# Optimization experiments

Hardware: AMD Instinct MI355X
Metric: run time of the kernel (lower is better)

Reference implementation:

```python
import jax, jax.numpy as jnp
import numpy as np

B, T, C = 1, 2048, 2048
H, KH, HD = 16, 4, 128  # n_head, n_kv_head, head_dim
ROPE_BASE = 10000.0


def setup_inputs() -> dict:
    key = jax.random.key(0)
    ks = jax.random.split(key, 5)
    s = 0.02
    return {
        "x": jax.random.normal(ks[0], (B, T, C), jnp.float32),
        "Wq": jax.random.normal(ks[1], (C, H * HD), jnp.float32) * s,
        "Wk": jax.random.normal(ks[2], (C, KH * HD), jnp.float32) * s,
        "Wv": jax.random.normal(ks[3], (C, KH * HD), jnp.float32) * s,
        "Wo": jax.random.normal(ks[4], (H * HD, C), jnp.float32) * s,
        "position_ids": jnp.arange(T, dtype=jnp.int32),
    }


def _rotate_half(a):
    h = a.shape[-1] // 2
    return jnp.concatenate([-a[..., h:], a[..., :h]], axis=-1)


def reference(x, Wq, Wk, Wv, Wo, position_ids):
    b, t, c = x.shape
    n_rep = H // KH
    # projections -> [B, heads, T, HD]
    q = (x @ Wq).reshape(b, t, H, HD).transpose(0, 2, 1, 3)
    k = (x @ Wk).reshape(b, t, KH, HD).transpose(0, 2, 1, 3)
    v = (x @ Wv).reshape(b, t, KH, HD).transpose(0, 2, 1, 3)
    # rotary embedding cache [T, HD]
    inv_freq = 1.0 / (ROPE_BASE ** (jnp.arange(0, HD, 2, dtype=jnp.float32) / HD))
    pos = jnp.arange(t, dtype=jnp.float32)
    freqs = pos[:, None] * inv_freq[None, :]
    emb = jnp.concatenate([freqs, freqs], axis=-1)
    cos = jnp.cos(emb)[position_ids][None, None]  # [1,1,T,HD]
    sin = jnp.sin(emb)[position_ids][None, None]
    q = q * cos + _rotate_half(q) * sin
    k = k * cos + _rotate_half(k) * sin
    # GQA: group query heads instead of materializing repeated K/V
    qg = q.reshape(b, KH, n_rep, t, HD)
    scale = jnp.float32(1.0 / np.sqrt(HD))
    scores = jnp.einsum('bgrtd,bgsd->bgrts', qg, k) * scale
    causal = jnp.tril(jnp.ones((t, t), dtype=bool))
    scores = jnp.where(causal, scores, jnp.float32(-1e30))
    p = jax.nn.softmax(scores, axis=-1)
    y = jnp.einsum('bgrts,bgsd->bgrtd', p, v)
    y = y.reshape(b, H, t, HD).transpose(0, 2, 1, 3).reshape(b, t, H * HD)
    return y @ Wo
```

## Files before the change

### kernel.cpp

```cpp
#include <hip/hip_runtime.h>

typedef unsigned short u16;
using bf16x8 = __attribute__((ext_vector_type(8))) short;
using f32x4  = __attribute__((ext_vector_type(4))) float;

#define GLD16(g, l)                                                            \
  __builtin_amdgcn_global_load_lds(                                            \
      (const __attribute__((address_space(1))) void*)(g),                      \
      (__attribute__((address_space(3))) void*)(l), 16, 0, 0)

__device__ __forceinline__ u16 f2b(float x) {
  union { float f; unsigned u; } v; v.f = x;
  unsigned r = v.u + 0x7FFF + ((v.u >> 16) & 1);
  return (u16)(r >> 16);
}
__device__ __forceinline__ float b2f(u16 x) {
  union { unsigned u; float f; } v; v.u = (unsigned)x << 16; return v.f;
}

__global__ void prep_kernel(const float* __restrict__ x,
                            const float* __restrict__ Wq,
                            const float* __restrict__ Wk,
                            const float* __restrict__ Wv,
                            const float* __restrict__ Wo,
                            const int* __restrict__ pos, u16* __restrict__ xb,
                            float2* __restrict__ tbl, u16* __restrict__ Wqkv_bt,
                            u16* __restrict__ Wo_bt) {
  __shared__ float tile[32][33];
  const int b = blockIdx.x, tid = threadIdx.x;
  if (b < 10240) {
    const int bx = b % 160, k0 = (b / 160) * 32;
    const int tx = tid & 31, ty = tid >> 5;
    const float* src; int srcN, n0s; u16* dst; int dstRow0;
    if (bx < 64)      { src = Wq; srcN = 2048; n0s = bx * 32;        dst = Wqkv_bt; dstRow0 = bx * 32; }
    else if (bx < 80) { src = Wk; srcN = 512;  n0s = (bx - 64) * 32; dst = Wqkv_bt; dstRow0 = 2048 + (bx - 64) * 32; }
    else if (bx < 96) { src = Wv; srcN = 512;  n0s = (bx - 80) * 32; dst = Wqkv_bt; dstRow0 = 2560 + (bx - 80) * 32; }
    else              { src = Wo; srcN = 2048; n0s = (bx - 96) * 32; dst = Wo_bt;   dstRow0 = (bx - 96) * 32; }
#pragma unroll
    for (int r = 0; r < 4; r++)
      tile[ty + r * 8][tx] = src[(size_t)(k0 + ty + r * 8) * srcN + n0s + tx];
    __syncthreads();
#pragma unroll
    for (int r = 0; r < 4; r++)
      dst[(size_t)(dstRow0 + ty + r * 8) * 2048 + k0 + tx] = f2b(tile[tx][ty + r * 8]);
  } else {
    int gid = (b - 10240) * 256 + tid;
    const float c0 = -0.015625f * 13.287712379549449f;
    for (int j = gid; j < 2048 * 64; j += 262144) {
      int t = j >> 6, d = j & 63;
      float ang = (float)pos[t] * exp2f((float)d * c0);
      tbl[j] = make_float2(cosf(ang), sinf(ang));
    }
    for (int i = gid; i < 1048576; i += 262144) {
      float4 v = ((const float4*)x)[i];
      ushort4 o;
      o.x = f2b(v.x); o.y = f2b(v.y); o.z = f2b(v.z); o.w = f2b(v.w);
      ((ushort4*)xb)[i] = o;
    }
  }
}

__global__ __launch_bounds__(256, 2)
void gemm_qkv_rope(const u16* __restrict__ A, const u16* __restrict__ Bt,
                   const float2* __restrict__ tbl, u16* __restrict__ Qb,
                   u16* __restrict__ Kb, u16* __restrict__ Vtb) {
  __shared__ u16 lds_[8][128 * 32];
  const int K = 2048;
  const int tid = threadIdx.x;
  const int lane = tid & 63;
  const int w = tid >> 6;
  const int wr = w >> 1, wc = w & 1;
  const int m0 = blockIdx.y * 128, n0 = blockIdx.x * 128;

  f32x4 acc[4][4] = {};

  const int srow = tid >> 2, skg = tid & 3;
  const u16* Ag0 = A + (size_t)(m0 + srow) * K + skg * 8;
  const u16* Ag1 = A + (size_t)(m0 + 64 + srow) * K + skg * 8;
  const u16* Bg0 = Bt + (size_t)(n0 + srow) * K + skg * 8;
  const u16* Bg1 = Bt + (size_t)(n0 + 64 + srow) * K + skg * 8;

  const int l0 = tid * 8, l1 = (256 + tid) * 8;
  u16 *pa0 = lds_[0], *pa1 = lds_[1], *pa2 = lds_[2], *pa3 = lds_[3];
  u16 *pb0 = lds_[4], *pb1 = lds_[5], *pb2 = lds_[6], *pb3 = lds_[7];

#define GSTAGE(k0v, pa, pb)                                                    \
  {                                                                            \
    GLD16(Ag0 + (k0v), (pa) + l0);                                             \
    GLD16(Ag1 + (k0v), (pa) + l1);                                             \
    GLD16(Bg0 + (k0v), (pb) + l0);                                             \
    GLD16(Bg1 + (k0v), (pb) + l1);                                             \
  }

  GSTAGE(0, pa0, pb0);
  GSTAGE(32, pa1, pb1);

  const int frow = lane & 15, fk = (lane >> 4) * 8;
  const int nk = K >> 5;

  for (int i = 0; i < nk; ++i) {
    if (i + 2 < nk) {
      GSTAGE((i + 2) * 32, pa2, pb2);
      asm volatile("s_waitcnt vmcnt(8)" ::: "memory");
    } else if (i + 1 < nk) {
      asm volatile("s_waitcnt vmcnt(4)" ::: "memory");
    } else {
      asm volatile("s_waitcnt vmcnt(0)" ::: "memory");
    }
    __builtin_amdgcn_s_barrier();
    __builtin_amdgcn_sched_barrier(0);
    bf16x8 av[4], bv[4];
#pragma unroll
    for (int m = 0; m < 4; m++)
      av[m] = *(const bf16x8*)(pa0 + (wr * 64 + m * 16 + frow) * 32 + fk);
#pragma unroll
    for (int n = 0; n < 4; n++)
      bv[n] = *(const bf16x8*)(pb0 + (wc * 64 + n * 16 + frow) * 32 + fk);
#pragma unroll
    for (int m = 0; m < 4; m++)
#pragma unroll
      for (int n = 0; n < 4; n++)
        acc[m][n] =
            __builtin_amdgcn_mfma_f32_16x16x32_bf16(av[m], bv[n], acc[m][n], 0, 0, 0);
    u16* t;
    t = pa0; pa0 = pa1; pa1 = pa2; pa2 = pa3; pa3 = t;
    t = pb0; pb0 = pb1; pb1 = pb2; pb2 = pb3; pb3 = t;
  }
#undef GSTAGE

  const int crow = (lane >> 4) * 4, ccol = lane & 15;
  __syncthreads();
  float* S = (float*)lds_;
#pragma unroll
  for (int m = 0; m < 4; m++)
#pragma unroll
    for (int n = 0; n < 4; n++)
#pragma unroll
      for (int r = 0; r < 4; r++)
        S[(wr * 64 + m * 16 + crow + r) * 128 + wc * 64 + n * 16 + ccol] =
            acc[m][n][r];
  __syncthreads();
  if (n0 < 2560) {
    const bool isQ = (n0 < 2048);
    u16* dst = isQ ? Qb + (size_t)(n0 >> 7) * 2048 * 128
                   : Kb + (size_t)((n0 - 2048) >> 7) * 2048 * 128;
    const float sgn = (wc == 0) ? -1.f : 1.f;
    const float qs = isQ ? 0.08838834764831845f : 1.0f;
#pragma unroll
    for (int m = 0; m < 4; m++)
#pragma unroll
      for (int n = 0; n < 4; n++)
#pragma unroll
        for (int r = 0; r < 4; r++) {
          int row = wr * 64 + m * 16 + crow + r;
          int col = wc * 64 + n * 16 + ccol;
          int t = m0 + row, d = col & 63;
          float2 cs = tbl[t * 64 + d];
          float val = acc[m][n][r] * cs.x + sgn * S[row * 128 + (col ^ 64)] * cs.y;
          dst[(size_t)t * 128 + col] = f2b(val * qs);
        }
  } else {
    const int g = (n0 - 2560) >> 7;
    u16* dst = Vtb + (size_t)g * 128 * 2048;
    const int d = tid >> 1, th = (tid & 1) * 64;
#pragma unroll
    for (int j = 0; j < 8; j++) {
      bf16x8 v;
#pragma unroll
      for (int e = 0; e < 8; e++) v[e] = (short)f2b(S[(th + j * 8 + e) * 128 + d]);
      *(bf16x8*)(dst + (size_t)d * 2048 + m0 + th + j * 8) = v;
    }
  }
}

__global__ __launch_bounds__(256, 2)
void gemm_bt_128(const u16* __restrict__ A, const u16* __restrict__ Bt,
                 float* __restrict__ C, int M, int N, int K) {
  __shared__ u16 As[4][128 * 32];
  __shared__ u16 Bs[4][128 * 32];
  const int tid = threadIdx.x;
  const int lane = tid & 63;
  const int w = tid >> 6;
  const int wr = w >> 1, wc = w & 1;
  const int m0 = blockIdx.y * 128, n0 = blockIdx.x * 128;

  f32x4 acc[4][4] = {};

  const int srow = tid >> 2, skg = tid & 3;
  const u16* Ag0 = A + (size_t)(m0 + srow) * K + skg * 8;
  const u16* Ag1 = A + (size_t)(m0 + 64 + srow) * K + skg * 8;
  const u16* Bg0 = Bt + (size_t)(n0 + srow) * K + skg * 8;
  const u16* Bg1 = Bt + (size_t)(n0 + 64 + srow) * K + skg * 8;

  const int l0 = tid * 8, l1 = (256 + tid) * 8;
  u16 *pa0 = As[0], *pa1 = As[1], *pa2 = As[2], *pa3 = As[3];
  u16 *pb0 = Bs[0], *pb1 = Bs[1], *pb2 = Bs[2], *pb3 = Bs[3];

#define GSTAGE(k0v, pa, pb)                                                    \
  {                                                                            \
    GLD16(Ag0 + (k0v), (pa) + l0);                                             \
    GLD16(Ag1 + (k0v), (pa) + l1);                                             \
    GLD16(Bg0 + (k0v), (pb) + l0);                                             \
    GLD16(Bg1 + (k0v), (pb) + l1);                                             \
  }

  GSTAGE(0, pa0, pb0);
  GSTAGE(32, pa1, pb1);

  const int frow = lane & 15, fk = (lane >> 4) * 8;
  const int nk = K >> 5;

  for (int i = 0; i < nk; ++i) {
    if (i + 2 < nk) {
      GSTAGE((i + 2) * 32, pa2, pb2);
      asm volatile("s_waitcnt vmcnt(8)" ::: "memory");
    } else if (i + 1 < nk) {
      asm volatile("s_waitcnt vmcnt(4)" ::: "memory");
    } else {
      asm volatile("s_waitcnt vmcnt(0)" ::: "memory");
    }
    __builtin_amdgcn_s_barrier();
    __builtin_amdgcn_sched_barrier(0);
    bf16x8 av[4], bv[4];
#pragma unroll
    for (int m = 0; m < 4; m++)
      av[m] = *(const bf16x8*)(pa0 + (wr * 64 + m * 16 + frow) * 32 + fk);
#pragma unroll
    for (int n = 0; n < 4; n++)
      bv[n] = *(const bf16x8*)(pb0 + (wc * 64 + n * 16 + frow) * 32 + fk);
#pragma unroll
    for (int m = 0; m < 4; m++)
#pragma unroll
      for (int n = 0; n < 4; n++)
        acc[m][n] =
            __builtin_amdgcn_mfma_f32_16x16x32_bf16(av[m], bv[n], acc[m][n], 0, 0, 0);
    u16* t;
    t = pa0; pa0 = pa1; pa1 = pa2; pa2 = pa3; pa3 = t;
    t = pb0; pb0 = pb1; pb1 = pb2; pb2 = pb3; pb3 = t;
  }
#undef GSTAGE

  const int crow = (lane >> 4) * 4, ccol = lane & 15;
#pragma unroll
  for (int m = 0; m < 4; m++)
#pragma unroll
    for (int n = 0; n < 4; n++)
#pragma unroll
      for (int r = 0; r < 4; r++)
        C[(size_t)(m0 + wr * 64 + m * 16 + crow + r) * N +
          (n0 + wc * 64 + n * 16 + ccol)] = acc[m][n][r];
}

__global__ __launch_bounds__(256, 3)
void attn_kernel(const u16* __restrict__ Qb, const u16* __restrict__ Kb,
                 const u16* __restrict__ Vtb, u16* __restrict__ op0,
                 u16* __restrict__ op1, u16* __restrict__ op2,
                 float* __restrict__ ml) {
  __shared__ u16 Ks[64 * 128];
  __shared__ u16 Vs[128 * 64];
  __shared__ u16 Ps[4][16 * 64];
  const int tid = threadIdx.x, lane = tid & 63, w = tid >> 6;
  const int h = blockIdx.y, g = h >> 2;
  const int z = blockIdx.z;
  const int frow = lane & 15, fgrp = lane >> 4;
  const int t0 = blockIdx.x;
  const int t1 = 31 - t0;
  const int c0 = (t0 >= z) ? (t0 - z) / 3 + 1 : 0;
  const int c1 = (t1 - z) / 3 + 1;
  const int nit = c0 + c1;
  u16* myOp = (z == 0) ? op0 : (z == 1) ? op1 : op2;

  const u16* Kg = Kb + (size_t)g * 2048 * 128;
  const u16* Vg = Vtb + (size_t)g * 128 * 2048;

#define STAGE(j0v)                                                             \
  {                                                                            \
    _Pragma("unroll")                                                          \
    for (int i = 0; i < 4; i++) {                                              \
      int p = tid + i * 256;                                                   \
      int kr = p >> 4, kc = (p & 15) ^ (kr & 7);                               \
      GLD16(Kg + (size_t)((j0v) + kr) * 128 + kc * 8, Ks + p * 8);             \
      int vr = p >> 3, vc = (p & 7) ^ (vr & 7);                                \
      GLD16(Vg + (size_t)vr * 2048 + (j0v) + vc * 8, Vs + p * 8);              \
    }                                                                          \
  }

#define FLUSH()                                                                \
  {                                                                            \
    _Pragma("unroll")                                                          \
    for (int r = 0; r < 4; r++) {                                              \
      float inv = lrow[r] > 0.f ? 1.0f / lrow[r] : 0.f;                        \
      int t = qw + fgrp * 4 + r;                                               \
      _Pragma("unroll")                                                        \
      for (int db = 0; db < 8; db++)                                           \
        myOp[(size_t)t * 2048 + h * 128 + db * 16 + frow] = f2b(o[db][r] * inv);\
      if (frow == 0) {                                                         \
        int mi = (((z * 16 + h) * 2048) + t) * 2;                              \
        ml[mi] = mrow[r]; ml[mi + 1] = lrow[r];                                \
      }                                                                        \
    }                                                                          \
  }

  int qw = t0 * 64 + w * 16;
  bf16x8 qf[4];
  {
    const u16* Qrow = Qb + ((size_t)h * 2048 + (qw + frow)) * 128 + fgrp * 8;
#pragma unroll
    for (int kf = 0; kf < 4; kf++) qf[kf] = *(const bf16x8*)(Qrow + kf * 32);
  }

  f32x4 o[8] = {};
  float mrow[4], lrow[4];
#pragma unroll
  for (int r = 0; r < 4; r++) { mrow[r] = -1e30f; lrow[r] = 0.f; }

  for (int it = 0; it < nit; ++it) {
    const int pass = (it < c0) ? 0 : 1;
    const int j = (pass == 0) ? z + 3 * it : z + 3 * (it - c0);
    STAGE(j * 64);
    if (it == c0) {
      FLUSH();
#pragma unroll
      for (int db = 0; db < 8; db++)
#pragma unroll
        for (int r = 0; r < 4; r++) o[db][r] = 0.f;
#pragma unroll
      for (int r = 0; r < 4; r++) { mrow[r] = -1e30f; lrow[r] = 0.f; }
      qw = t1 * 64 + w * 16;
      const u16* Qrow = Qb + ((size_t)h * 2048 + (qw + frow)) * 128 + fgrp * 8;
#pragma unroll
      for (int kf = 0; kf < 4; kf++) qf[kf] = *(const bf16x8*)(Qrow + kf * 32);
    }
    __syncthreads();
    const bool diag = (pass == 0) ? (j == t0) : (j == t1);

    f32x4 sc[4] = {};
#pragma unroll
    for (int c = 0; c < 4; c++)
#pragma unroll
      for (int kf = 0; kf < 4; kf++) {
        int row = c * 16 + frow;
        bf16x8 kv = *(const bf16x8*)(
            &Ks[row * 128 + ((kf * 4 + fgrp) ^ (row & 7)) * 8]);
        sc[c] = __builtin_amdgcn_mfma_f32_16x16x32_bf16(qf[kf], kv, sc[c], 0, 0, 0);
      }
    if (diag) {
#pragma unroll
      for (int c = 0; c < 4; c++) {
        int jj = c * 16 + frow;
#pragma unroll
        for (int r = 0; r < 4; r++)
          if (jj > (w * 16 + fgrp * 4 + r)) sc[c][r] = -1e30f;
      }
    }
    float pm[4];
#pragma unroll
    for (int r = 0; r < 4; r++)
      pm[r] = fmaxf(fmaxf(sc[0][r], sc[1][r]), fmaxf(sc[2][r], sc[3][r]));
#pragma unroll
    for (int off = 1; off < 16; off <<= 1)
#pragma unroll
      for (int r = 0; r < 4; r++) pm[r] = fmaxf(pm[r], __shfl_xor(pm[r], off, 64));
    bool nd = false;
#pragma unroll
    for (int r = 0; r < 4; r++) nd = nd || (pm[r] > mrow[r] + 8.f);
    if (__any(nd)) {
#pragma unroll
      for (int r = 0; r < 4; r++) {
        float mn = fmaxf(mrow[r], pm[r]);
        float alpha = __expf(mrow[r] - mn);
        mrow[r] = mn;
        lrow[r] *= alpha;
#pragma unroll
        for (int db = 0; db < 8; db++) o[db][r] *= alpha;
      }
    }
    float rs[4];
#pragma unroll
    for (int r = 0; r < 4; r++) {
      float s = 0.f;
#pragma unroll
      for (int c = 0; c < 4; c++) { sc[c][r] = __expf(sc[c][r] - mrow[r]); s += sc[c][r]; }
      rs[r] = s;
    }
#pragma unroll
    for (int off = 1; off < 16; off <<= 1)
#pragma unroll
      for (int r = 0; r < 4; r++) rs[r] += __shfl_xor(rs[r], off, 64);
#pragma unroll
    for (int r = 0; r < 4; r++) lrow[r] += rs[r];
    u16* Pw = Ps[w];
#pragma unroll
    for (int c = 0; c < 4; c++)
#pragma unroll
      for (int r = 0; r < 4; r++) {
        int row = fgrp * 4 + r, col = c * 16 + frow;
        Pw[row * 64 + (((col >> 3) ^ row) & 7) * 8 + (col & 7)] = f2b(sc[c][r]);
      }
    asm volatile("s_waitcnt lgkmcnt(0)" ::: "memory");
    bf16x8 pf[2];
#pragma unroll
    for (int ks = 0; ks < 2; ks++)
      pf[ks] = *(const bf16x8*)(
          &Pw[frow * 64 + ((ks * 4 + fgrp) ^ (frow & 7)) * 8]);
#pragma unroll
    for (int db = 0; db < 8; db++)
#pragma unroll
      for (int ks = 0; ks < 2; ks++) {
        int row = db * 16 + frow;
        bf16x8 vf = *(const bf16x8*)(
            &Vs[row * 64 + ((ks * 4 + fgrp) ^ (row & 7)) * 8]);
        o[db] = __builtin_amdgcn_mfma_f32_16x16x32_bf16(pf[ks], vf, o[db], 0, 0, 0);
      }
    __syncthreads();
  }
  FLUSH();
#undef STAGE
#undef FLUSH
}

__global__ void attn_combine_kernel(const u16* __restrict__ op0,
                                    const u16* __restrict__ op1,
                                    const u16* __restrict__ op2,
                                    const float* __restrict__ ml,
                                    u16* __restrict__ Y) {
  int u = blockIdx.x * blockDim.x + threadIdx.x;
  int t = u >> 4, h = u & 15;
  float m0 = ml[((0 + h) * 2048 + t) * 2],       l0 = ml[((0 + h) * 2048 + t) * 2 + 1];
  float m1 = ml[((16 + h) * 2048 + t) * 2],      l1 = ml[((16 + h) * 2048 + t) * 2 + 1];
  float m2 = ml[((32 + h) * 2048 + t) * 2],      l2 = ml[((32 + h) * 2048 + t) * 2 + 1];
  float m = fmaxf(fmaxf(m0, m1), m2);
  float w0 = __expf(m0 - m) * l0, w1 = __expf(m1 - m) * l1, w2 = __expf(m2 - m) * l2;
  float inv = 1.0f / (w0 + w1 + w2);
  w0 *= inv; w1 *= inv; w2 *= inv;
  size_t base = (size_t)t * 2048 + h * 128;
#pragma unroll
  for (int i = 0; i < 16; i++) {
    bf16x8 a = *(const bf16x8*)(op0 + base + i * 8);
    bf16x8 b = *(const bf16x8*)(op1 + base + i * 8);
    bf16x8 c = *(const bf16x8*)(op2 + base + i * 8);
    bf16x8 out;
#pragma unroll
    for (int jj = 0; jj < 8; jj++)
      out[jj] = (short)f2b(w0 * b2f((u16)a[jj]) + w1 * b2f((u16)b[jj]) +
                           w2 * b2f((u16)c[jj]));
    *(bf16x8*)(Y + base + i * 8) = out;
  }
}

extern "C" void kernel_launch(void* const* d_in, const int* in_sizes, int n_in,
                              void* d_out, int out_size, void* d_ws,
                              size_t ws_size, hipStream_t stream) {
  const float* x  = (const float*)d_in[0];
  const float* Wq = (const float*)d_in[1];
  const float* Wk = (const float*)d_in[2];
  const float* Wv = (const float*)d_in[3];
  const float* Wo = (const float*)d_in[4];
  const int* pos  = (const int*)d_in[5];
  float* out = (float*)d_out;
  char* ws = (char*)d_ws;

  u16* xb      = (u16*)(ws + 0);
  u16* Wqkv_bt = (u16*)(ws + 8388608);
  u16* Wo_bt   = (u16*)(ws + 20971520);
  float2* tbl  = (float2*)(ws + 29360128);
  u16* Yb      = (u16*)(ws + 31457280);
  u16* Op2     = (u16*)(ws + 39845888);
  u16* Qb      = (u16*)(ws + 54525952);
  u16* Kb      = (u16*)(ws + 62914560);
  u16* Vtb     = (u16*)(ws + 67108864);
  u16* Op0     = (u16*)(ws + 0);
  u16* Op1     = (u16*)(ws + 8388608);
  float* ml    = (float*)(ws + 16777216);

  prep_kernel<<<11264, 256, 0, stream>>>(x, Wq, Wk, Wv, Wo, pos, xb, tbl,
                                         Wqkv_bt, Wo_bt);

  gemm_qkv_rope<<<dim3(24, 16), 256, 0, stream>>>(xb, Wqkv_bt, tbl, Qb, Kb, Vtb);

  attn_kernel<<<dim3(16, 16, 3), 256, 0, stream>>>(Qb, Kb, Vtb, Op0, Op1, Op2, ml);
  attn_combine_kernel<<<128, 256, 0, stream>>>(Op0, Op1, Op2, ml, Yb);

  gemm_bt_128<<<dim3(16, 16), 256, 0, stream>>>(Yb, Wo_bt, out, 2048, 2048, 2048);
}
```

Baseline: 243.1 us.

## Double query rows per attention wave and split KV four ways

Each wave now processes 32 query rows (two 16-row MFMA fragments) against each staged K/V tile, so a block covers 128 queries and every LDS K/V load is reused twice. The KV split along the sequence goes from 3 to 4 partitions, with a fourth partial output buffer and a 4-way combine, and the grid becomes 8x16x4. The point is to halve K/V staging and LDS traffic per unit of attention work. In exchange register pressure roughly doubles (launch bounds drop to 2 blocks per SM), more diagonal tiles need masking, and the combine reads an extra partial buffer. The workspace layout is also reorganised.

```diff
diff --git a/kernel.cpp b/kernel.cpp
--- a/kernel.cpp
+++ b/kernel.cpp
@@ -251,25 +251,25 @@
           (n0 + wc * 64 + n * 16 + ccol)] = acc[m][n][r];
 }
 
-__global__ __launch_bounds__(256, 3)
+__global__ __launch_bounds__(256, 2)
 void attn_kernel(const u16* __restrict__ Qb, const u16* __restrict__ Kb,
                  const u16* __restrict__ Vtb, u16* __restrict__ op0,
                  u16* __restrict__ op1, u16* __restrict__ op2,
-                 float* __restrict__ ml) {
+                 u16* __restrict__ op3, float* __restrict__ ml) {
   __shared__ u16 Ks[64 * 128];
   __shared__ u16 Vs[128 * 64];
-  __shared__ u16 Ps[4][16 * 64];
+  __shared__ u16 Ps[4][32 * 64];
   const int tid = threadIdx.x, lane = tid & 63, w = tid >> 6;
   const int h = blockIdx.y, g = h >> 2;
   const int z = blockIdx.z;
   const int frow = lane & 15, fgrp = lane >> 4;
   const int t0 = blockIdx.x;
-  const int t1 = 31 - t0;
-  const int c0 = (t0 >= z) ? (t0 - z) / 3 + 1 : 0;
-  const int c1 = (t1 - z) / 3 + 1;
+  const int t1 = 15 - t0;
+  const int c0 = (2 * t0 + 1 >= z) ? (2 * t0 + 1 - z) / 4 + 1 : 0;
+  const int c1 = (2 * t1 + 1 - z) / 4 + 1;
   const int nit = c0 + c1;
-  u16* myOp = (z == 0) ? op0 : (z == 1) ? op1 : op2;
-
+
+  u16* myOp = (z == 0) ? op0 : (z == 1) ? op1 : (z == 2) ? op2 : op3;
   const u16* Kg = Kb + (size_t)g * 2048 * 128;
   const u16* Vg = Vtb + (size_t)g * 128 * 2048;
 
@@ -288,53 +288,72 @@
 #define FLUSH()                                                                \
   {                                                                            \
     _Pragma("unroll")                                                          \
-    for (int r = 0; r < 4; r++) {                                              \
-      float inv = lrow[r] > 0.f ? 1.0f / lrow[r] : 0.f;                        \
-      int t = qw + fgrp * 4 + r;                                               \
+    for (int rg = 0; rg < 2; rg++)                                             \
       _Pragma("unroll")                                                        \
-      for (int db = 0; db < 8; db++)                                           \
-        myOp[(size_t)t * 2048 + h * 128 + db * 16 + frow] = f2b(o[db][r] * inv);\
-      if (frow == 0) {                                                         \
-        int mi = (((z * 16 + h) * 2048) + t) * 2;                              \
-        ml[mi] = mrow[r]; ml[mi + 1] = lrow[r];                                \
+      for (int r = 0; r < 4; r++) {                                            \
+        float lr = rg ? lrow1[r] : lrow0[r];                                   \
+        float mr = rg ? mrow1[r] : mrow0[r];                                   \
+        float inv = lr > 0.f ? 1.0f / lr : 0.f;                                \
+        int t = qw + rg * 16 + fgrp * 4 + r;                                   \
+        _Pragma("unroll")                                                      \
+        for (int db = 0; db < 8; db++) {                                       \
+          float ov = rg ? o1[db][r] : o0[db][r];                               \
+          myOp[(size_t)t * 2048 + h * 128 + db * 16 + frow] = f2b(ov * inv);   \
+        }                                                                      \
+        if (frow == 0) {                                                       \
+          int mi = (((z * 16 + h) * 2048) + t) * 2;                            \
+          ml[mi] = mr; ml[mi + 1] = lr;                                        \
+        }                                                                      \
       }                                                                        \
-    }                                                                          \
-  }
-
-  int qw = t0 * 64 + w * 16;
-  bf16x8 qf[4];
+  }
+
+  int qw = t0 * 128 + w * 32;
+  bf16x8 qf0[4], qf1[4];
   {
-    const u16* Qrow = Qb + ((size_t)h * 2048 + (qw + frow)) * 128 + fgrp * 8;
-#pragma unroll
-    for (int kf = 0; kf < 4; kf++) qf[kf] = *(const bf16x8*)(Qrow + kf * 32);
-  }
-
-  f32x4 o[8] = {};
-  float mrow[4], lrow[4];
-#pragma unroll
-  for (int r = 0; r < 4; r++) { mrow[r] = -1e30f; lrow[r] = 0.f; }
+    const u16* Qr0 = Qb + ((size_t)h * 2048 + (qw + frow)) * 128 + fgrp * 8;
+    const u16* Qr1 = Qb + ((size_t)h * 2048 + (qw + 16 + frow)) * 128 + fgrp * 8;
+#pragma unroll
+    for (int kf = 0; kf < 4; kf++) {
+      qf0[kf] = *(const bf16x8*)(Qr0 + kf * 32);
+      qf1[kf] = *(const bf16x8*)(Qr1 + kf * 32);
+    }
+  }
+
+  f32x4 o0[8] = {}, o1[8] = {};
+  float mrow0[4], lrow0[4], mrow1[4], lrow1[4];
+#pragma unroll
+  for (int r = 0; r < 4; r++) {
+    mrow0[r] = -1e30f; lrow0[r] = 0.f; mrow1[r] = -1e30f; lrow1[r] = 0.f;
+  }
 
   for (int it = 0; it < nit; ++it) {
     const int pass = (it < c0) ? 0 : 1;
-    const int j = (pass == 0) ? z + 3 * it : z + 3 * (it - c0);
+    const int j = (pass == 0) ? z + 4 * it : z + 4 * (it - c0);
     STAGE(j * 64);
     if (it == c0) {
       FLUSH();
 #pragma unroll
       for (int db = 0; db < 8; db++)
 #pragma unroll
-        for (int r = 0; r < 4; r++) o[db][r] = 0.f;
-#pragma unroll
-      for (int r = 0; r < 4; r++) { mrow[r] = -1e30f; lrow[r] = 0.f; }
-      qw = t1 * 64 + w * 16;
-      const u16* Qrow = Qb + ((size_t)h * 2048 + (qw + frow)) * 128 + fgrp * 8;
-#pragma unroll
-      for (int kf = 0; kf < 4; kf++) qf[kf] = *(const bf16x8*)(Qrow + kf * 32);
+        for (int r = 0; r < 4; r++) { o0[db][r] = 0.f; o1[db][r] = 0.f; }
+#pragma unroll
+      for (int r = 0; r < 4; r++) {
+        mrow0[r] = -1e30f; lrow0[r] = 0.f; mrow1[r] = -1e30f; lrow1[r] = 0.f;
+      }
+      qw = t1 * 128 + w * 32;
+      const u16* Qr0 = Qb + ((size_t)h * 2048 + (qw + frow)) * 128 + fgrp * 8;
+      const u16* Qr1 = Qb + ((size_t)h * 2048 + (qw + 16 + frow)) * 128 + fgrp * 8;
+#pragma unroll
+      for (int kf = 0; kf < 4; kf++) {
+        qf0[kf] = *(const bf16x8*)(Qr0 + kf * 32);
+        qf1[kf] = *(const bf16x8*)(Qr1 + kf * 32);
+      }
     }
     __syncthreads();
-    const bool diag = (pass == 0) ? (j == t0) : (j == t1);
-
-    f32x4 sc[4] = {};
+    const int qt = (pass == 0) ? t0 : t1;
+    const bool diag = (j >= 2 * qt);
+
+    f32x4 sc0[4] = {}, sc1[4] = {};
 #pragma unroll
     for (int c = 0; c < 4; c++)
 #pragma unroll
@@ -342,67 +361,89 @@
         int row = c * 16 + frow;
         bf16x8 kv = *(const bf16x8*)(
             &Ks[row * 128 + ((kf * 4 + fgrp) ^ (row & 7)) * 8]);
-        sc[c] = __builtin_amdgcn_mfma_f32_16x16x32_bf16(qf[kf], kv, sc[c], 0, 0, 0);
+        sc0[c] = __builtin_amdgcn_mfma_f32_16x16x32_bf16(qf0[kf], kv, sc0[c], 0, 0, 0);
+        sc1[c] = __builtin_amdgcn_mfma_f32_16x16x32_bf16(qf1[kf], kv, sc1[c], 0, 0, 0);
       }
     if (diag) {
 #pragma unroll
       for (int c = 0; c < 4; c++) {
-        int jj = c * 16 + frow;
-#pragma unroll
-        for (int r = 0; r < 4; r++)
-          if (jj > (w * 16 + fgrp * 4 + r)) sc[c][r] = -1e30f;
-      }
-    }
-    float pm[4];
+        int jg = j * 64 + c * 16 + frow;
+#pragma unroll
+        for (int r = 0; r < 4; r++) {
+          if (jg > qw + fgrp * 4 + r) sc0[c][r] = -1e30f;
+          if (jg > qw + 16 + fgrp * 4 + r) sc1[c][r] = -1e30f;
+        }
+      }
+    }
+    float pm0[4], pm1[4];
+#pragma unroll
+    for (int r = 0; r < 4; r++) {
+      pm0[r] = fmaxf(fmaxf(sc0[0][r], sc0[1][r]), fmaxf(sc0[2][r], sc0[3][r]));
+      pm1[r] = fmaxf(fmaxf(sc1[0][r], sc1[1][r]), fmaxf(sc1[2][r], sc1[3][r]));
+    }
+#pragma unroll
+    for (int off = 1; off < 16; off <<= 1)
+#pragma unroll
+      for (int r = 0; r < 4; r++) {
+        pm0[r] = fmaxf(pm0[r], __shfl_xor(pm0[r], off, 64));
+        pm1[r] = fmaxf(pm1[r], __shfl_xor(pm1[r], off, 64));
+      }
+    bool nd = false;
 #pragma unroll
     for (int r = 0; r < 4; r++)
-      pm[r] = fmaxf(fmaxf(sc[0][r], sc[1][r]), fmaxf(sc[2][r], sc[3][r]));
+      nd = nd || (pm0[r] > mrow0[r] + 8.f) || (pm1[r] > mrow1[r] + 8.f);
+    if (__any(nd)) {
+#pragma unroll
+      for (int r = 0; r < 4; r++) {
+        float mn0 = fmaxf(mrow0[r], pm0[r]);
+        float a0 = __expf(mrow0[r] - mn0);
+        mrow0[r] = mn0; lrow0[r] *= a0;
+        float mn1 = fmaxf(mrow1[r], pm1[r]);
+        float a1 = __expf(mrow1[r] - mn1);
+        mrow1[r] = mn1; lrow1[r] *= a1;
+#pragma unroll
+        for (int db = 0; db < 8; db++) { o0[db][r] *= a0; o1[db][r] *= a1; }
+      }
+    }
+    float rs0[4], rs1[4];
+#pragma unroll
+    for (int r = 0; r < 4; r++) {
+      float s0 = 0.f, s1 = 0.f;
+#pragma unroll
+      for (int c = 0; c < 4; c++) {
+        sc0[c][r] = __expf(sc0[c][r] - mrow0[r]); s0 += sc0[c][r];
+        sc1[c][r] = __expf(sc1[c][r] - mrow1[r]); s1 += sc1[c][r];
+      }
+      rs0[r] = s0; rs1[r] = s1;
+    }
 #pragma unroll
     for (int off = 1; off < 16; off <<= 1)
 #pragma unroll
-      for (int r = 0; r < 4; r++) pm[r] = fmaxf(pm[r], __shfl_xor(pm[r], off, 64));
-    bool nd = false;
-#pragma unroll
-    for (int r = 0; r < 4; r++) nd = nd || (pm[r] > mrow[r] + 8.f);
-    if (__any(nd)) {
-#pragma unroll
       for (int r = 0; r < 4; r++) {
-        float mn = fmaxf(mrow[r], pm[r]);
-        float alpha = __expf(mrow[r] - mn);
-        mrow[r] = mn;
-        lrow[r] *= alpha;
-#pragma unroll
-        for (int db = 0; db < 8; db++) o[db][r] *= alpha;
-      }
-    }
-    float rs[4];
-#pragma unroll
-    for (int r = 0; r < 4; r++) {
-      float s = 0.f;
-#pragma unroll
-      for (int c = 0; c < 4; c++) { sc[c][r] = __expf(sc[c][r] - mrow[r]); s += sc[c][r]; }
-      rs[r] = s;
-    }
-#pragma unroll
-    for (int off = 1; off < 16; off <<= 1)
-#pragma unroll
-      for (int r = 0; r < 4; r++) rs[r] += __shfl_xor(rs[r], off, 64);
-#pragma unroll
-    for (int r = 0; r < 4; r++) lrow[r] += rs[r];
+        rs0[r] += __shfl_xor(rs0[r], off, 64);
+        rs1[r] += __shfl_xor(rs1[r], off, 64);
+      }
+#pragma unroll
+    for (int r = 0; r < 4; r++) { lrow0[r] += rs0[r]; lrow1[r] += rs1[r]; }
     u16* Pw = Ps[w];
 #pragma unroll
     for (int c = 0; c < 4; c++)
 #pragma unroll
       for (int r = 0; r < 4; r++) {
-        int row = fgrp * 4 + r, col = c * 16 + frow;
-        Pw[row * 64 + (((col >> 3) ^ row) & 7) * 8 + (col & 7)] = f2b(sc[c][r]);
+        int col = c * 16 + frow;
+        int row0 = fgrp * 4 + r, row1 = 16 + fgrp * 4 + r;
+        Pw[row0 * 64 + (((col >> 3) ^ row0) & 7) * 8 + (col & 7)] = f2b(sc0[c][r]);
+        Pw[row1 * 64 + (((col >> 3) ^ row1) & 7) * 8 + (col & 7)] = f2b(sc1[c][r]);
       }
     asm volatile("s_waitcnt lgkmcnt(0)" ::: "memory");
-    bf16x8 pf[2];
-#pragma unroll
-    for (int ks = 0; ks < 2; ks++)
-      pf[ks] = *(const bf16x8*)(
+    bf16x8 pf0[2], pf1[2];
+#pragma unroll
+    for (int ks = 0; ks < 2; ks++) {
+      pf0[ks] = *(const bf16x8*)(
           &Pw[frow * 64 + ((ks * 4 + fgrp) ^ (frow & 7)) * 8]);
+      pf1[ks] = *(const bf16x8*)(
+          &Pw[(16 + frow) * 64 + ((ks * 4 + fgrp) ^ (frow & 7)) * 8]);
+    }
 #pragma unroll
     for (int db = 0; db < 8; db++)
 #pragma unroll
@@ -410,7 +451,8 @@
         int row = db * 16 + frow;
         bf16x8 vf = *(const bf16x8*)(
             &Vs[row * 64 + ((ks * 4 + fgrp) ^ (row & 7)) * 8]);
-        o[db] = __builtin_amdgcn_mfma_f32_16x16x32_bf16(pf[ks], vf, o[db], 0, 0, 0);
+        o0[db] = __builtin_amdgcn_mfma_f32_16x16x32_bf16(pf0[ks], vf, o0[db], 0, 0, 0);
+        o1[db] = __builtin_amdgcn_mfma_f32_16x16x32_bf16(pf1[ks], vf, o1[db], 0, 0, 0);
       }
     __syncthreads();
   }
@@ -422,28 +464,32 @@
 __global__ void attn_combine_kernel(const u16* __restrict__ op0,
                                     const u16* __restrict__ op1,
                                     const u16* __restrict__ op2,
+                                    const u16* __restrict__ op3,
                                     const float* __restrict__ ml,
                                     u16* __restrict__ Y) {
   int u = blockIdx.x * blockDim.x + threadIdx.x;
   int t = u >> 4, h = u & 15;
-  float m0 = ml[((0 + h) * 2048 + t) * 2],       l0 = ml[((0 + h) * 2048 + t) * 2 + 1];
-  float m1 = ml[((16 + h) * 2048 + t) * 2],      l1 = ml[((16 + h) * 2048 + t) * 2 + 1];
-  float m2 = ml[((32 + h) * 2048 + t) * 2],      l2 = ml[((32 + h) * 2048 + t) * 2 + 1];
-  float m = fmaxf(fmaxf(m0, m1), m2);
-  float w0 = __expf(m0 - m) * l0, w1 = __expf(m1 - m) * l1, w2 = __expf(m2 - m) * l2;
-  float inv = 1.0f / (w0 + w1 + w2);
-  w0 *= inv; w1 *= inv; w2 *= inv;
+  float m0 = ml[((0 + h) * 2048 + t) * 2],  l0 = ml[((0 + h) * 2048 + t) * 2 + 1];
+  float m1 = ml[((16 + h) * 2048 + t) * 2], l1 = ml[((16 + h) * 2048 + t) * 2 + 1];
+  float m2 = ml[((32 + h) * 2048 + t) * 2], l2 = ml[((32 + h) * 2048 + t) * 2 + 1];
+  float m3 = ml[((48 + h) * 2048 + t) * 2], l3 = ml[((48 + h) * 2048 + t) * 2 + 1];
+  float m = fmaxf(fmaxf(m0, m1), fmaxf(m2, m3));
+  float w0 = __expf(m0 - m) * l0, w1 = __expf(m1 - m) * l1;
+  float w2 = __expf(m2 - m) * l2, w3 = __expf(m3 - m) * l3;
+  float inv = 1.0f / (w0 + w1 + w2 + w3);
+  w0 *= inv; w1 *= inv; w2 *= inv; w3 *= inv;
   size_t base = (size_t)t * 2048 + h * 128;
 #pragma unroll
   for (int i = 0; i < 16; i++) {
     bf16x8 a = *(const bf16x8*)(op0 + base + i * 8);
     bf16x8 b = *(const bf16x8*)(op1 + base + i * 8);
     bf16x8 c = *(const bf16x8*)(op2 + base + i * 8);
+    bf16x8 d = *(const bf16x8*)(op3 + base + i * 8);
     bf16x8 out;
 #pragma unroll
     for (int jj = 0; jj < 8; jj++)
       out[jj] = (short)f2b(w0 * b2f((u16)a[jj]) + w1 * b2f((u16)b[jj]) +
-                           w2 * b2f((u16)c[jj]));
+                           w2 * b2f((u16)c[jj]) + w3 * b2f((u16)d[jj]));
     *(bf16x8*)(Y + base + i * 8) = out;
   }
 }
@@ -459,27 +505,30 @@
   const int* pos  = (const int*)d_in[5];
   float* out = (float*)d_out;
   char* ws = (char*)d_ws;
-
-  u16* xb      = (u16*)(ws + 0);
-  u16* Wqkv_bt = (u16*)(ws + 8388608);
-  u16* Wo_bt   = (u16*)(ws + 20971520);
-  float2* tbl  = (float2*)(ws + 29360128);
-  u16* Yb      = (u16*)(ws + 31457280);
-  u16* Op2     = (u16*)(ws + 39845888);
-  u16* Qb      = (u16*)(ws + 54525952);
-  u16* Kb      = (u16*)(ws + 62914560);
-  u16* Vtb     = (u16*)(ws + 67108864);
-  u16* Op0     = (u16*)(ws + 0);
-  u16* Op1     = (u16*)(ws + 8388608);
-  float* ml    = (float*)(ws + 16777216);
+  const size_t MB = 1048576;
+
+  u16* Wo_bt   = (u16*)(ws + 0);
+  u16* Qb      = (u16*)(ws + 8 * MB);
+  u16* Kb      = (u16*)(ws + 16 * MB);
+  u16* Vtb     = (u16*)(ws + 18 * MB);
+  u16* Op0     = (u16*)(ws + 20 * MB);
+  u16* Op1     = (u16*)(ws + 28 * MB);
+  u16* Op2     = (u16*)(ws + 36 * MB);
+  u16* Op3     = (u16*)(ws + 44 * MB);
+  float* ml    = (float*)(ws + 52 * MB);
+  u16* Yb      = (u16*)(ws + 53 * MB);
+  u16* xb      = (u16*)(ws + 20 * MB);
+  u16* Wqkv_bt = (u16*)(ws + 28 * MB);
+  float2* tbl  = (float2*)(ws + 41 * MB);
 
   prep_kernel<<<11264, 256, 0, stream>>>(x, Wq, Wk, Wv, Wo, pos, xb, tbl,
                                          Wqkv_bt, Wo_bt);
 
   gemm_qkv_rope<<<dim3(24, 16), 256, 0, stream>>>(xb, Wqkv_bt, tbl, Qb, Kb, Vtb);
 
-  attn_kernel<<<dim3(16, 16, 3), 256, 0, stream>>>(Qb, Kb, Vtb, Op0, Op1, Op2, ml);
-  attn_combine_kernel<<<128, 256, 0, stream>>>(Op0, Op1, Op2, ml, Yb);
+  attn_kernel<<<dim3(8, 16, 4), 256, 0, stream>>>(Qb, Kb, Vtb, Op0, Op1, Op2,
+                                                  Op3, ml);
+  attn_combine_kernel<<<128, 256, 0, stream>>>(Op0, Op1, Op2, Op3, ml, Yb);
 
   gemm_bt_128<<<dim3(16, 16), 256, 0, stream>>>(Yb, Wo_bt, out, 2048, 2048, 2048);
 }
```

New measurement: 247.4 us. Within noise of the previous version (+1.8%).
